# Performance work log

Hardware: AMD Instinct MI355X
Metric: run time of the kernel (lower is better)

## Reference

```python
import jax, jax.numpy as jnp
import numpy as np

WIDTH, DEPTH = 2048, 8
TIME_MOD = 30 * DEPTH + 2  # 242


def setup_inputs() -> dict:
    key = jax.random.key(0)
    ks = jax.random.split(key, 7)
    s = float(np.sqrt(1.0 / WIDTH))
    so = float(np.sqrt(1.0 / (WIDTH + DEPTH + 1)))
    return {
        "x": jax.random.normal(ks[0], (WIDTH,), dtype=jnp.float32),
        "weights": jax.random.uniform(ks[1], (WIDTH, WIDTH, DEPTH), minval=-s, maxval=s, dtype=jnp.float32),
        "output_weights": jax.random.uniform(ks[2], (WIDTH, DEPTH + 1), minval=-so, maxval=so, dtype=jnp.float32),
        "state": jax.random.uniform(ks[3], (WIDTH, DEPTH + 1), dtype=jnp.float32),  # relu outputs >= 0
        "stored_activations": jax.random.uniform(ks[4], (WIDTH, DEPTH + 1, TIME_MOD), dtype=jnp.float32),
        "stored_gradiets": jax.random.normal(ks[5], (WIDTH, DEPTH), dtype=jnp.float32),
        "output_gradient": jax.random.normal(ks[6], (WIDTH, DEPTH + 1, TIME_MOD), dtype=jnp.float32),
        "time": 7,
    }


def reference(x, weights, output_weights, state, stored_activations, stored_gradiets, output_gradient, time):
    width, dp1 = state.shape
    depth = dp1 - 1
    mod = 30 * depth + 2
    dt = state.dtype

    # recurrent state update: state[w,d] = relu(sum_i weights[i,w,d] * state_prev[i,d])
    hidden = jax.nn.relu(jnp.einsum("iwd,id->wd", weights, state[:, :depth]))
    state = jnp.concatenate([x[:, None], hidden], axis=1)  # (W, depth+1)
    output = jnp.sum(output_weights * state)

    # scatter into circular buffers at slot `time` (static int)
    sa = stored_activations.at[:, :, time].set(state)
    og = output_gradient.at[:, :, time].set(output_weights)

    # stored gradients: loop over a reads only OLD stored_gradiets[:, a+1] -> vectorizable
    a = np.arange(depth - 1)  # a = 0 .. depth-2 (static indices)
    t_idx = (time - 2 * depth + 2 * (a + 1)) % mod  # (depth-1,)
    relu_m = (sa[:, a + 2, (t_idx + 1) % mod] > 0).astype(dt)  # (W, depth-1)
    contrib = jnp.einsum("ija,ja->ia", weights[:, :, 1:depth], stored_gradiets[:, 1:depth])
    sg_head = relu_m * contrib + og[:, a + 1, t_idx]  # (W, depth-1)
    sg_last = og[:, depth, time]  # a == depth-1 branch (time_index == time)
    sg = jnp.concatenate([sg_head, sg_last[:, None]], axis=1)  # (W, depth)

    output_weights_gradient = state

    # weight eligibility traces (uses UPDATED sa and UPDATED sg)
    aa = np.arange(depth)
    tia = (time - 2 * depth + 2 * (aa + 1)) % mod  # (depth,)
    relu_g = (sa[:, aa + 1, tia] > 0).astype(dt)  # (W, depth)
    act_prev = sa[:, aa, (tia - 1) % mod]  # (W, depth)
    gradients = act_prev[:, None, :] * (sg * relu_g)[None, :, :]  # (W, W, depth)

    return output, state, sa, sg, og, gradients, output_weights_gradient
```

## Files before the change

kernel.cpp:

```cpp
#include <hip/hip_runtime.h>

#define MOD 242

static constexpr long long OFF_STATE = 1;
static constexpr long long OFF_SA    = 18433;
static constexpr long long OFF_SG    = 4478977;
static constexpr long long OFF_OG    = 4495361;
static constexpr long long OFF_GRAD  = 8955905;
static constexpr long long OFF_OWG   = 42510337;

#define WS_HID  0
#define WS_CON  524288
#define WS_COL  786432
#define WS_ROW  802816
#define WS_OUTP 819200

template <int CTRL, int RM>
__device__ __forceinline__ float dppadd(float x) {
  int t = __builtin_amdgcn_update_dpp(0, __float_as_int(x), CTRL, RM, 0xF, true);
  return x + __int_as_float(t);
}
__device__ __forceinline__ float wave_sum_dpp(float x) {
  x = dppadd<0x111, 0xF>(x);
  x = dppadd<0x112, 0xF>(x);
  x = dppadd<0x114, 0xF>(x);
  x = dppadd<0x118, 0xF>(x);
  x = dppadd<0x142, 0xA>(x);
  x = dppadd<0x143, 0xC>(x);
  return x;
}

__global__ __launch_bounds__(256) void k_matvec(
    const float* __restrict__ weights, const float* __restrict__ state,
    const float* __restrict__ sgrad, float* __restrict__ ws)
{
  const int b    = blockIdx.x;
  const int iblk = b & 31;
  const int wblk = b >> 5;
  const int i0   = iblk * 64;
  const int w0   = wblk * 128;
  const int tid  = threadIdx.x;
  const int wv   = tid >> 6;
  const int l    = tid & 63;
  const int wgrp = wv >> 1;
  const int dh   = wv & 1;
  const int w    = w0 + wgrp * 64 + l;

  __shared__ __align__(16) float state_lds[64 * 8];
  __shared__ __align__(16) float cl[4][64][4];

  for (int idx = tid; idx < 64 * 8; idx += 256)
    state_lds[idx] = state[(size_t)(i0 + (idx >> 3)) * 9 + (idx & 7)];
  __syncthreads();

  const float4 sg4 = *(const float4*)&sgrad[(size_t)w * 8 + dh * 4];
  float4 h4 = make_float4(0.f, 0.f, 0.f, 0.f);
  const float* wp = weights + ((size_t)i0 * 2048 + w) * 8 + dh * 4;

  #pragma unroll 4
  for (int ii = 0; ii < 64; ++ii) {
    const float4 w4 = *(const float4*)wp;
    wp += 16384;
    const float4 s4 = *(const float4*)&state_lds[ii * 8 + dh * 4];

    h4.x = fmaf(w4.x, s4.x, h4.x);
    h4.y = fmaf(w4.y, s4.y, h4.y);
    h4.z = fmaf(w4.z, s4.z, h4.z);
    h4.w = fmaf(w4.w, s4.w, h4.w);

    float vx = wave_sum_dpp(w4.x * sg4.x);
    float vy = wave_sum_dpp(w4.y * sg4.y);
    float vz = wave_sum_dpp(w4.z * sg4.z);
    float vw = wave_sum_dpp(w4.w * sg4.w);
    if (l == 63)
      *(float4*)&cl[wv][ii][0] = make_float4(vx, vy, vz, vw);
  }

  *(float4*)&ws[WS_HID + ((size_t)iblk * 2048 + w) * 8 + dh * 4] = h4;

  __syncthreads();
  {
    const int ii = tid >> 2, q = tid & 3;
    const float c0 = cl[0][ii][q] + cl[2][ii][q];
    const float c1 = cl[1][ii][q] + cl[3][ii][q];
    const size_t base = WS_CON + ((size_t)wblk * 2048 + i0 + ii) * 8;
    ws[base + q]     = c0;
    ws[base + 4 + q] = c1;
  }
}

__global__ __launch_bounds__(256) void k_copy2(
    const float* __restrict__ a, float* __restrict__ da,
    const float* __restrict__ b, float* __restrict__ db)
{
  const int i = blockIdx.x * 256 + threadIdx.x;
  da[i] = a[i];
  db[i] = b[i];
}

__global__ __launch_bounds__(64) void k_finalize(
    const float* __restrict__ x, const float* __restrict__ ow,
    const float* __restrict__ sa_in, const float* __restrict__ og_in,
    const int* __restrict__ timep, float* __restrict__ ws, float* __restrict__ out)
{
  const int r = blockIdx.x * 64 + threadIdx.x;
  const int t = *timep;

  float hid[8] = {0,0,0,0,0,0,0,0};
  {
    const float4* hp = (const float4*)&ws[WS_HID + (size_t)r * 8];
    #pragma unroll
    for (int ib = 0; ib < 32; ++ib) {
      const float4 pa = hp[(size_t)ib * 4096];
      const float4 pb = hp[(size_t)ib * 4096 + 1];
      hid[0] += pa.x; hid[1] += pa.y; hid[2] += pa.z; hid[3] += pa.w;
      hid[4] += pb.x; hid[5] += pb.y; hid[6] += pb.z; hid[7] += pb.w;
    }
  }
  float con[8] = {0,0,0,0,0,0,0,0};
  {
    const float4* cp = (const float4*)&ws[WS_CON + (size_t)r * 8];
    #pragma unroll
    for (int wb = 0; wb < 16; ++wb) {
      const float4 pa = cp[(size_t)wb * 4096];
      const float4 pb = cp[(size_t)wb * 4096 + 1];
      con[0] += pa.x; con[1] += pa.y; con[2] += pa.z; con[3] += pa.w;
      con[4] += pb.x; con[5] += pb.y; con[6] += pb.z; con[7] += pb.w;
    }
  }

  float s[9];
  s[0] = x[r];
  #pragma unroll
  for (int d = 0; d < 8; ++d) s[d + 1] = fmaxf(hid[d], 0.f);

  float owr[9];
  #pragma unroll
  for (int c = 0; c < 9; ++c) owr[c] = ow[(size_t)r * 9 + c];

  float p = 0.f;
  #pragma unroll
  for (int c = 0; c < 9; ++c) {
    out[OFF_STATE + (size_t)r * 9 + c] = s[c];
    out[OFF_OWG   + (size_t)r * 9 + c] = s[c];
    out[OFF_SA + ((size_t)r * 9 + c) * MOD + t] = s[c];
    out[OFF_OG + ((size_t)r * 9 + c) * MOD + t] = owr[c];
    p = fmaf(owr[c], s[c], p);
  }
  #pragma unroll
  for (int m = 1; m < 64; m <<= 1) p += __shfl_xor(p, m);
  if (threadIdx.x == 0) ws[WS_OUTP + blockIdx.x] = p;

  float sg[8];
  #pragma unroll
  for (int a = 0; a < 7; ++a) {
    const int ti = (t + 2 * a - 14 + MOD) % MOD;
    const int tm = (ti + 1) % MOD;
    const float av  = (tm == t) ? s[a + 2] : sa_in[((size_t)r * 9 + a + 2) * MOD + tm];
    const float ogv = (ti == t) ? owr[a + 1] : og_in[((size_t)r * 9 + a + 1) * MOD + ti];
    sg[a] = (av > 0.f ? con[a + 1] : 0.f) + ogv;
  }
  sg[7] = owr[8];
  #pragma unroll
  for (int a = 0; a < 8; ++a) out[OFF_SG + (size_t)r * 8 + a] = sg[a];

  #pragma unroll
  for (int aa = 0; aa < 8; ++aa) {
    const int ti = (t + 2 * aa - 14 + MOD) % MOD;
    const int tp = (ti - 1 + MOD) % MOD;
    const float rv = (ti == t) ? s[aa + 1] : sa_in[((size_t)r * 9 + aa + 1) * MOD + ti];
    const float ap = (tp == t) ? s[aa]     : sa_in[((size_t)r * 9 + aa) * MOD + tp];
    ws[WS_COL + r * 8 + aa] = (rv > 0.f) ? sg[aa] : 0.f;
    ws[WS_ROW + r * 8 + aa] = ap;
  }
}

__global__ __launch_bounds__(256) void k_grad(
    const float* __restrict__ ws, float* __restrict__ out)
{
  const int i = blockIdx.x;
  const int tid = threadIdx.x;
  if (i == 0 && tid == 0) {
    float s = 0.f;
    #pragma unroll
    for (int k = 0; k < 32; ++k) s += ws[WS_OUTP + k];
    out[0] = s;
  }
  const float rf = ws[WS_ROW + i * 8 + (tid & 7)];
  float* o = out + OFF_GRAD + (size_t)i * 16384;
  const float* cf = ws + WS_COL;
  #pragma unroll 4
  for (int k = 0; k < 64; ++k) {
    const int e = k * 256 + tid;
    o[e] = rf * cf[e];
  }
}

extern "C" void kernel_launch(void* const* d_in, const int* in_sizes, int n_in,
                              void* d_out, int out_size, void* d_ws, size_t ws_size,
                              hipStream_t stream)
{
  (void)in_sizes; (void)n_in; (void)out_size; (void)ws_size;
  const float* x     = (const float*)d_in[0];
  const float* wts   = (const float*)d_in[1];
  const float* ow    = (const float*)d_in[2];
  const float* st    = (const float*)d_in[3];
  const float* sa_in = (const float*)d_in[4];
  const float* sgrad = (const float*)d_in[5];
  const float* og_in = (const float*)d_in[6];
  const int*   timep = (const int*)d_in[7];
  float* out = (float*)d_out;
  float* ws  = (float*)d_ws;

  k_matvec<<<512, 256, 0, stream>>>(wts, st, sgrad, ws);
  k_copy2<<<17424, 256, 0, stream>>>(sa_in, out + OFF_SA, og_in, out + OFF_OG);
  k_finalize<<<32, 64, 0, stream>>>(x, ow, sa_in, og_in, timep, ws, out);
  k_grad<<<2048, 256, 0, stream>>>(ws, out);
}
```

Before: 342.7 us.

## Fuse buffer copies into matvec, split finalize reduction, vectorize gradient stores

Drops the separate copy kernel and has each matvec block copy an 8712-element slice of the stored activations and output gradient buffers, so the copy runs alongside the weight streaming. The finalize kernel now uses four lanes per row with shuffle reductions across 128 blocks instead of 32, which raises parallelism for the partial-sum gathers. The gradient kernel writes aligned float4 stores, handling the 3-element offset at the start of each row separately. The fused copy lengthens the matvec blocks and may contend with the weight stream for bandwidth.

```diff
diff --git a/kernel.cpp b/kernel.cpp
--- a/kernel.cpp
+++ b/kernel.cpp
@@ -32,7 +32,9 @@
 
 __global__ __launch_bounds__(256) void k_matvec(
     const float* __restrict__ weights, const float* __restrict__ state,
-    const float* __restrict__ sgrad, float* __restrict__ ws)
+    const float* __restrict__ sgrad, const float* __restrict__ sa_in,
+    const float* __restrict__ og_in, float* __restrict__ ws,
+    float* __restrict__ out)
 {
   const int b    = blockIdx.x;
   const int iblk = b & 31;
@@ -87,15 +89,14 @@
     ws[base + q]     = c0;
     ws[base + 4 + q] = c1;
   }
-}
-
-__global__ __launch_bounds__(256) void k_copy2(
-    const float* __restrict__ a, float* __restrict__ da,
-    const float* __restrict__ b, float* __restrict__ db)
-{
-  const int i = blockIdx.x * 256 + threadIdx.x;
-  da[i] = a[i];
-  db[i] = b[i];
+
+  {
+    const int e0 = b * 8712;
+    for (int e = tid; e < 8712; e += 256) {
+      out[OFF_SA + (size_t)(e0 + e)] = sa_in[e0 + e];
+      out[OFF_OG + (size_t)(e0 + e)] = og_in[e0 + e];
+    }
+  }
 }
 
 __global__ __launch_bounds__(64) void k_finalize(
@@ -103,16 +104,19 @@
     const float* __restrict__ sa_in, const float* __restrict__ og_in,
     const int* __restrict__ timep, float* __restrict__ ws, float* __restrict__ out)
 {
-  const int r = blockIdx.x * 64 + threadIdx.x;
-  const int t = *timep;
+  const int tid = threadIdx.x;
+  const int q   = tid & 3;
+  const int r   = blockIdx.x * 16 + (tid >> 2);
+  const int t   = *timep;
 
   float hid[8] = {0,0,0,0,0,0,0,0};
   {
     const float4* hp = (const float4*)&ws[WS_HID + (size_t)r * 8];
     #pragma unroll
-    for (int ib = 0; ib < 32; ++ib) {
-      const float4 pa = hp[(size_t)ib * 4096];
-      const float4 pb = hp[(size_t)ib * 4096 + 1];
+    for (int k = 0; k < 8; ++k) {
+      const size_t ib = (size_t)(q + 4 * k);
+      const float4 pa = hp[ib * 4096];
+      const float4 pb = hp[ib * 4096 + 1];
       hid[0] += pa.x; hid[1] += pa.y; hid[2] += pa.z; hid[3] += pa.w;
       hid[4] += pb.x; hid[5] += pb.y; hid[6] += pb.z; hid[7] += pb.w;
     }
@@ -121,58 +125,69 @@
   {
     const float4* cp = (const float4*)&ws[WS_CON + (size_t)r * 8];
     #pragma unroll
-    for (int wb = 0; wb < 16; ++wb) {
-      const float4 pa = cp[(size_t)wb * 4096];
-      const float4 pb = cp[(size_t)wb * 4096 + 1];
+    for (int k = 0; k < 4; ++k) {
+      const size_t wb = (size_t)(q + 4 * k);
+      const float4 pa = cp[wb * 4096];
+      const float4 pb = cp[wb * 4096 + 1];
       con[0] += pa.x; con[1] += pa.y; con[2] += pa.z; con[3] += pa.w;
       con[4] += pb.x; con[5] += pb.y; con[6] += pb.z; con[7] += pb.w;
     }
   }
-
-  float s[9];
-  s[0] = x[r];
   #pragma unroll
-  for (int d = 0; d < 8; ++d) s[d + 1] = fmaxf(hid[d], 0.f);
-
-  float owr[9];
-  #pragma unroll
-  for (int c = 0; c < 9; ++c) owr[c] = ow[(size_t)r * 9 + c];
+  for (int m = 1; m <= 2; m <<= 1) {
+    #pragma unroll
+    for (int d = 0; d < 8; ++d) {
+      hid[d] += __shfl_xor(hid[d], m);
+      con[d] += __shfl_xor(con[d], m);
+    }
+  }
 
   float p = 0.f;
-  #pragma unroll
-  for (int c = 0; c < 9; ++c) {
-    out[OFF_STATE + (size_t)r * 9 + c] = s[c];
-    out[OFF_OWG   + (size_t)r * 9 + c] = s[c];
-    out[OFF_SA + ((size_t)r * 9 + c) * MOD + t] = s[c];
-    out[OFF_OG + ((size_t)r * 9 + c) * MOD + t] = owr[c];
-    p = fmaf(owr[c], s[c], p);
+  if (q == 0) {
+    float s[9];
+    s[0] = x[r];
+    #pragma unroll
+    for (int d = 0; d < 8; ++d) s[d + 1] = fmaxf(hid[d], 0.f);
+
+    float owr[9];
+    #pragma unroll
+    for (int c = 0; c < 9; ++c) owr[c] = ow[(size_t)r * 9 + c];
+
+    #pragma unroll
+    for (int c = 0; c < 9; ++c) {
+      out[OFF_STATE + (size_t)r * 9 + c] = s[c];
+      out[OFF_OWG   + (size_t)r * 9 + c] = s[c];
+      out[OFF_SA + ((size_t)r * 9 + c) * MOD + t] = s[c];
+      out[OFF_OG + ((size_t)r * 9 + c) * MOD + t] = owr[c];
+      p = fmaf(owr[c], s[c], p);
+    }
+
+    float sg[8];
+    #pragma unroll
+    for (int a = 0; a < 7; ++a) {
+      const int ti = (t + 2 * a - 14 + MOD) % MOD;
+      const int tm = (ti + 1) % MOD;
+      const float av  = (tm == t) ? s[a + 2] : sa_in[((size_t)r * 9 + a + 2) * MOD + tm];
+      const float ogv = (ti == t) ? owr[a + 1] : og_in[((size_t)r * 9 + a + 1) * MOD + ti];
+      sg[a] = (av > 0.f ? con[a + 1] : 0.f) + ogv;
+    }
+    sg[7] = owr[8];
+    #pragma unroll
+    for (int a = 0; a < 8; ++a) out[OFF_SG + (size_t)r * 8 + a] = sg[a];
+
+    #pragma unroll
+    for (int aa = 0; aa < 8; ++aa) {
+      const int ti = (t + 2 * aa - 14 + MOD) % MOD;
+      const int tp = (ti - 1 + MOD) % MOD;
+      const float rv = (ti == t) ? s[aa + 1] : sa_in[((size_t)r * 9 + aa + 1) * MOD + ti];
+      const float ap = (tp == t) ? s[aa]     : sa_in[((size_t)r * 9 + aa) * MOD + tp];
+      ws[WS_COL + r * 8 + aa] = (rv > 0.f) ? sg[aa] : 0.f;
+      ws[WS_ROW + r * 8 + aa] = ap;
+    }
   }
   #pragma unroll
   for (int m = 1; m < 64; m <<= 1) p += __shfl_xor(p, m);
-  if (threadIdx.x == 0) ws[WS_OUTP + blockIdx.x] = p;
-
-  float sg[8];
-  #pragma unroll
-  for (int a = 0; a < 7; ++a) {
-    const int ti = (t + 2 * a - 14 + MOD) % MOD;
-    const int tm = (ti + 1) % MOD;
-    const float av  = (tm == t) ? s[a + 2] : sa_in[((size_t)r * 9 + a + 2) * MOD + tm];
-    const float ogv = (ti == t) ? owr[a + 1] : og_in[((size_t)r * 9 + a + 1) * MOD + ti];
-    sg[a] = (av > 0.f ? con[a + 1] : 0.f) + ogv;
-  }
-  sg[7] = owr[8];
-  #pragma unroll
-  for (int a = 0; a < 8; ++a) out[OFF_SG + (size_t)r * 8 + a] = sg[a];
-
-  #pragma unroll
-  for (int aa = 0; aa < 8; ++aa) {
-    const int ti = (t + 2 * aa - 14 + MOD) % MOD;
-    const int tp = (ti - 1 + MOD) % MOD;
-    const float rv = (ti == t) ? s[aa + 1] : sa_in[((size_t)r * 9 + aa + 1) * MOD + ti];
-    const float ap = (tp == t) ? s[aa]     : sa_in[((size_t)r * 9 + aa) * MOD + tp];
-    ws[WS_COL + r * 8 + aa] = (rv > 0.f) ? sg[aa] : 0.f;
-    ws[WS_ROW + r * 8 + aa] = ap;
-  }
+  if (tid == 0) ws[WS_OUTP + blockIdx.x] = p;
 }
 
 __global__ __launch_bounds__(256) void k_grad(
@@ -183,17 +198,28 @@
   if (i == 0 && tid == 0) {
     float s = 0.f;
     #pragma unroll
-    for (int k = 0; k < 32; ++k) s += ws[WS_OUTP + k];
+    for (int k = 0; k < 128; ++k) s += ws[WS_OUTP + k];
     out[0] = s;
   }
-  const float rf = ws[WS_ROW + i * 8 + (tid & 7)];
+  const float4* rp = (const float4*)&ws[WS_ROW + (size_t)i * 8];
+  const float4 rA = rp[0];
+  const float4 rB = rp[1];
+  const float4 rf4 = (tid & 1)
+      ? make_float4(rB.w, rA.x, rA.y, rA.z)
+      : make_float4(rA.w, rB.x, rB.y, rB.z);
+  const float* cf = ws + WS_COL;
   float* o = out + OFF_GRAD + (size_t)i * 16384;
-  const float* cf = ws + WS_COL;
+
   #pragma unroll 4
-  for (int k = 0; k < 64; ++k) {
-    const int e = k * 256 + tid;
-    o[e] = rf * cf[e];
-  }
+  for (int v = tid; v < 4095; v += 256) {
+    const int e0 = 4 * v + 3;
+    const float c0 = cf[e0], c1 = cf[e0 + 1], c2 = cf[e0 + 2], c3 = cf[e0 + 3];
+    *(float4*)&o[e0] = make_float4(rf4.x * c0, rf4.y * c1, rf4.z * c2, rf4.w * c3);
+  }
+  if (tid == 0) o[0] = rA.x * cf[0];
+  if (tid == 1) o[1] = rA.y * cf[1];
+  if (tid == 2) o[2] = rA.z * cf[2];
+  if (tid == 3) o[16383] = rB.w * cf[16383];
 }
 
 extern "C" void kernel_launch(void* const* d_in, const int* in_sizes, int n_in,
@@ -212,8 +238,7 @@
   float* out = (float*)d_out;
   float* ws  = (float*)d_ws;
 
-  k_matvec<<<512, 256, 0, stream>>>(wts, st, sgrad, ws);
-  k_copy2<<<17424, 256, 0, stream>>>(sa_in, out + OFF_SA, og_in, out + OFF_OG);
-  k_finalize<<<32, 64, 0, stream>>>(x, ow, sa_in, og_in, timep, ws, out);
+  k_matvec<<<512, 256, 0, stream>>>(wts, st, sgrad, sa_in, og_in, ws, out);
+  k_finalize<<<128, 64, 0, stream>>>(x, ow, sa_in, og_in, timep, ws, out);
   k_grad<<<2048, 256, 0, stream>>>(ws, out);
 }
```

Result: slower. 364.8 us (+6.4%).
